# Optimization experiments

Hardware: AMD Instinct MI355X
Metric: run time of the kernel (lower is better)

The kernel has to match this reference:

```python
import jax, jax.numpy as jnp
import numpy as np

BS, C, H, W = 8, 128, 64, 64
CH = C // 2  # proj output channels


def setup_inputs() -> dict:
    key = jax.random.key(0)
    ks = jax.random.split(key, 8)
    s = 1.0 / np.sqrt(C)
    return {
        "tgt": jax.random.normal(ks[0], (BS, C, H, W), dtype=jnp.float32),
        "ref": jax.random.normal(ks[1], (BS, C, H, W), dtype=jnp.float32),
        "W_tgt": jax.random.normal(ks[2], (CH, C), dtype=jnp.float32) * s,
        "b_tgt": jax.random.normal(ks[3], (CH,), dtype=jnp.float32) * s,
        "W_ref": jax.random.normal(ks[4], (CH, C), dtype=jnp.float32) * s,
        "b_ref": jax.random.normal(ks[5], (CH,), dtype=jnp.float32) * s,
        "W_out": jax.random.normal(ks[6], (C, C), dtype=jnp.float32) * s,
        "b_out": jax.random.normal(ks[7], (C,), dtype=jnp.float32) * s,
    }


def reference(tgt, ref, W_tgt, b_tgt, W_ref, b_ref, W_out, b_out):
    bs, c, h, w = tgt.shape
    n = h * w
    # 1x1 conv == per-pixel matmul over channels; flatten spatial to tokens
    tgt_f = tgt.reshape(bs, c, n)              # [bs, c, n]
    ref_f = ref.reshape(bs, c, n)              # [bs, c, n]
    # att_tgt: [bs, n, c/2] ; att_ref: [bs, c/2, n] (ReLU after proj)
    att_tgt = jax.nn.relu(jnp.einsum('bcn,oc->bno', tgt_f, W_tgt) + b_tgt)
    att_ref = jax.nn.relu(jnp.einsum('bcn,oc->bon', ref_f, W_ref) + b_ref[None, :, None])
    pre_att = jnp.einsum('bnd,bdm->bnm', att_tgt, att_ref)   # [bs, n, n]
    att = jax.nn.softmax(pre_att, axis=-1)
    # fused tokens: [bs, n, c] = att @ ref_tokens
    fused = jnp.einsum('bnm,bcm->bnc', att, ref_f)
    fused = fused.transpose(0, 2, 1).reshape(bs, c, h, w)
    # output gate: 1x1 conv on tgt (no activation), elementwise mul
    att_out = jnp.einsum('bcn,oc->bon', tgt_f, W_out) + b_out[None, :, None]
    fused = fused * att_out.reshape(bs, c, h, w)
    return fused
```

## Files before the change

### kernel.cpp

```cpp
#include <hip/hip_runtime.h>

typedef __attribute__((ext_vector_type(8))) _Float16 f16x8;
typedef __attribute__((ext_vector_type(4))) float f32x4;
typedef __attribute__((ext_vector_type(16))) float f32x16;
typedef __attribute__((ext_vector_type(2))) unsigned u32x2;

constexpr int kC  = 128;
constexpr int kCH = 64;
constexpr int kN  = 4096;
constexpr float kLog2e = 1.4426950408889634f;

__device__ __forceinline__ unsigned pkrtz(float a, float b) {
    union { __fp16 __attribute__((ext_vector_type(2))) v; unsigned u; } cv;
    cv.v = __builtin_amdgcn_cvt_pkrtz(a, b);
    return cv.u;
}

__device__ __forceinline__ float x2(float x) {
    return __builtin_amdgcn_exp2f(x);
}

__device__ __forceinline__ float hadd2(unsigned u) {
    union { unsigned v; _Float16 h[2]; } c; c.v = u;
    return (float)c.h[0] + (float)c.h[1];
}

__device__ __forceinline__ u32x2 pl32(unsigned a, unsigned b) {
    return __builtin_amdgcn_permlane32_swap(a, b, false, false);
}
__device__ __forceinline__ u32x2 pl32x(float v) {
    float c;
    asm("v_mov_b32 %0, %1" : "=&v"(c) : "v"(v));
    union { float f; unsigned u; } a, b2; a.f = v; b2.f = c;
    return pl32(a.u, b2.u);
}
__device__ __forceinline__ float uf(unsigned u) {
    union { unsigned v; float f; } c; c.v = u; return c.f;
}

__device__ __forceinline__ void g2l16(const unsigned short* g, unsigned short* l) {
    __builtin_amdgcn_global_load_lds(
        (const __attribute__((address_space(1))) unsigned int*)(g),
        (__attribute__((address_space(3))) unsigned int*)(l),
        16, 0, 0);
}

__global__ __launch_bounds__(256, 2) void proj_fused(
    const float* __restrict__ tgt, const float* __restrict__ ref,
    const float* __restrict__ Wt, const float* __restrict__ Wr,
    const float* __restrict__ Wo, const float* __restrict__ bt,
    const float* __restrict__ br, const float* __restrict__ bo,
    unsigned short* __restrict__ Qw, unsigned short* __restrict__ Kw,
    unsigned short* __restrict__ Vw, float* __restrict__ Gw)
{
    __shared__ __align__(16) unsigned short Xs[2][64 * 128];
    const int t = threadIdx.x;
    const int sl2 = blockIdx.y >> 3;
    const int b = blockIdx.y & 7;
    const int tok0 = blockIdx.x << 7;

    const int w = t >> 6, lane = t & 63;
    const int lg = (lane >> 4) & 3, lm = lane & 15;

    const float* X = sl2 ? ref : tgt;
    const float* Xb0 = X + ((size_t)b * kC) * kN + tok0;
    unsigned short* Vout = Vw + ((size_t)b * kC) * kN + tok0;

    const float* Wqk  = sl2 ? Wr : Wt;
    const float* bqk  = sl2 ? br : bt;
    const float scale = sl2 ? 1.0f : kLog2e;

    f16x8 wfq[4];
    float bq[4];
    {
        const int ocb = w * 16;
        #pragma unroll
        for (int ks = 0; ks < 4; ++ks) {
            const float* wp = Wqk + (size_t)(ocb + lm) * kC + ks * 32 + lg * 8;
            f32x4 f0 = *(const f32x4*)wp;
            f32x4 f1 = *(const f32x4*)(wp + 4);
            union { f16x8 h; uint4 u; } cv;
            cv.u = make_uint4(pkrtz(f0[0] * scale, f0[1] * scale),
                              pkrtz(f0[2] * scale, f0[3] * scale),
                              pkrtz(f1[0] * scale, f1[1] * scale),
                              pkrtz(f1[2] * scale, f1[3] * scale));
            wfq[ks] = cv.h;
        }
        #pragma unroll
        for (int r = 0; r < 4; ++r) bq[r] = bqk[ocb + lg * 4 + r] * scale;
    }

    f16x8 wfg[2][4];
    float bg[2][4];
    if (sl2 == 0) {
        const int ocb = w * 32;
        #pragma unroll
        for (int ot = 0; ot < 2; ++ot) {
            const int oc = ocb + ot * 16 + lm;
            #pragma unroll
            for (int ks = 0; ks < 4; ++ks) {
                const float* wp = Wo + (size_t)oc * kC + ks * 32 + lg * 8;
                f32x4 f0 = *(const f32x4*)wp;
                f32x4 f1 = *(const f32x4*)(wp + 4);
                union { f16x8 h; uint4 u; } cv;
                cv.u = make_uint4(pkrtz(f0[0], f0[1]), pkrtz(f0[2], f0[3]),
                                  pkrtz(f1[0], f1[1]), pkrtz(f1[2], f1[3]));
                wfg[ot][ks] = cv.h;
            }
            #pragma unroll
            for (int r = 0; r < 4; ++r) bg[ot][r] = bo[ocb + ot * 16 + lg * 4 + r];
        }
    }

    const int tk4 = (t & 15) * 4;
    const int c8  = (t >> 4) * 8;

    auto loadX = [&](int toff, f32x4* xv) {
        #pragma unroll
        for (int j = 0; j < 8; ++j)
            xv[j] = *(const f32x4*)(Xb0 + (size_t)(c8 + j) * kN + toff + tk4);
    };
    auto stageX = [&](const f32x4* xv, unsigned short* Xsb, int toff) {
        if (sl2 == 1) {
            #pragma unroll
            for (int j = 0; j < 8; ++j)
                *(uint2*)(Vout + (size_t)(c8 + j) * kN + toff + tk4) =
                    make_uint2(pkrtz(xv[j][0], xv[j][1]), pkrtz(xv[j][2], xv[j][3]));
        }
        #pragma unroll
        for (int s = 0; s < 4; ++s) {
            const int tok = tk4 + s;
            const int cc = (c8 >> 3) ^ (tok & 7);
            uint4 pk;
            pk.x = pkrtz(xv[0][s], xv[1][s]);
            pk.y = pkrtz(xv[2][s], xv[3][s]);
            pk.z = pkrtz(xv[4][s], xv[5][s]);
            pk.w = pkrtz(xv[6][s], xv[7][s]);
            *(uint4*)(Xsb + tok * 128 + cc * 8) = pk;
        }
    };
    auto compute = [&](const unsigned short* Xsb, int tokb) {
        unsigned short* outp = (sl2 ? Kw : Qw) + ((size_t)b * kN + tokb) * kCH;
        float* Gb = Gw + ((size_t)b * kC) * kN + tokb;
        const int ocq = w * 16;
        const int ocg = w * 32;
        #pragma unroll
        for (int ns = 0; ns < 4; ++ns) {
            const int tok = ns * 16 + lm;
            f16x8 xf[4];
            #pragma unroll
            for (int ks = 0; ks < 4; ++ks)
                xf[ks] = *(const f16x8*)(Xsb + tok * 128 +
                                         (((ks * 4 + lg) ^ (tok & 7)) << 3));
            {
                f32x4 acc = {bq[0], bq[1], bq[2], bq[3]};
                #pragma unroll
                for (int ks = 0; ks < 4; ++ks)
                    acc = __builtin_amdgcn_mfma_f32_16x16x32_f16(wfq[ks], xf[ks], acc, 0, 0, 0);
                uint2 pk;
                pk.x = pkrtz(fmaxf(acc[0], 0.f), fmaxf(acc[1], 0.f));
                pk.y = pkrtz(fmaxf(acc[2], 0.f), fmaxf(acc[3], 0.f));
                *(uint2*)(outp + (size_t)tok * kCH + ocq + lg * 4) = pk;
            }
            if (sl2 == 0) {
                #pragma unroll
                for (int ot = 0; ot < 2; ++ot) {
                    f32x4 acc = {bg[ot][0], bg[ot][1], bg[ot][2], bg[ot][3]};
                    #pragma unroll
                    for (int ks = 0; ks < 4; ++ks)
                        acc = __builtin_amdgcn_mfma_f32_16x16x32_f16(wfg[ot][ks], xf[ks], acc, 0, 0, 0);
                    #pragma unroll
                    for (int r = 0; r < 4; ++r)
                        Gb[(size_t)(ocg + ot * 16 + lg * 4 + r) * kN + tok] = acc[r];
                }
            }
        }
    };

    f32x4 xv[8], xw[8];
    loadX(0, xv);
    stageX(xv, Xs[0], 0);
    __syncthreads();
    loadX(64, xw);
    compute(Xs[0], tok0);
    stageX(xw, Xs[1], 64);
    __syncthreads();
    compute(Xs[1], tok0 + 64);
}

__global__ __launch_bounds__(256, 2) void flash12_kernel(
    const unsigned short* __restrict__ Qw,
    const unsigned short* __restrict__ Kw,
    const unsigned short* __restrict__ Vw,
    const float* __restrict__ Gw,
    float* __restrict__ out)
{
    __shared__ __align__(16) unsigned short Ks[2][64 * 64];
    __shared__ __align__(16) unsigned short Vs[3][128 * 64];
    __shared__ float2 mlb[4][32];

    const int t = threadIdx.x;
    const int b  = blockIdx.x & 7;
    const int n0 = (blockIdx.x >> 3) << 6;
    const int w = t >> 6, lane = t & 63;
    const int qg = w >> 1, kh = w & 1;
    const int lq = lane & 31, hh = lane >> 5;
    const int n0q = n0 + qg * 32 + lq;

    const unsigned short* Qb = Qw + ((size_t)b * kN + n0q) * kCH;
    const unsigned short* Kb = Kw + ((size_t)b * kN) * kCH;
    const unsigned short* Vb = Vw + ((size_t)b * kC) * kN;

    f16x8 qf[4];
    #pragma unroll
    for (int st = 0; st < 4; ++st)
        qf[st] = *(const f16x8*)(Qb + st * 16 + hh * 8);

    const int srow = t >> 3, scol = t & 7;
    const int sco  = (scol ^ (srow & 7)) << 3;
    const int wv   = t >> 6;

    int ka[4];
    #pragma unroll
    for (int st = 0; st < 4; ++st)
        ka[st] = (kh * 32 + lq) * 64 + (((2 * st + hh) ^ (lq & 7)) << 3);
    int va[4][2];
    #pragma unroll
    for (int cb = 0; cb < 4; ++cb)
        #pragma unroll
        for (int s = 0; s < 2; ++s)
            va[cb][s] = (cb * 32 + lq) * 64 + (((kh * 4 + 2 * s + hh) ^ (lq & 7)) << 3);

    f32x16 O[4];
    #pragma unroll
    for (int cb = 0; cb < 4; ++cb)
        #pragma unroll
        for (int r = 0; r < 16; ++r) O[cb][r] = 0.f;
    float L = 0.f, m_run = 0.f;

    f16x8 pfp[2];
    {
        union { uint4 u; f16x8 h; } z;
        z.u = make_uint4(0u, 0u, 0u, 0u);
        pfp[0] = z.h; pfp[1] = z.h;
    }

    auto stage = [&](unsigned short* Kd, unsigned short* Vd, int m0) {
        g2l16(Kb + (size_t)(m0 + srow) * kCH + sco,      Kd + wv * 512);
        g2l16(Kb + (size_t)(m0 + 32 + srow) * kCH + sco, Kd + 2048 + wv * 512);
        #pragma unroll
        for (int j = 0; j < 4; ++j)
            g2l16(Vb + (size_t)(32 * j + srow) * kN + m0 + sco,
                  Vd + j * 2048 + wv * 512);
    };

    unsigned short *Kt = Ks[0], *Kn = Ks[1];
    unsigned short *Vp = Vs[2], *Vt = Vs[0], *Vn = Vs[1];
    stage(Kt, Vt, 0);

    for (int kt = 0; kt < kN / 64; ++kt) {
        __syncthreads();
        if (kt + 1 < kN / 64) stage(Kn, Vn, (kt + 1) << 6);

        f32x16 sa;
        #pragma unroll
        for (int r = 0; r < 16; ++r) sa[r] = 0.f;
        __builtin_amdgcn_s_setprio(1);
        #pragma unroll
        for (int st = 0; st < 4; ++st) {
            f16x8 kf = *(const f16x8*)(Kt + ka[st]);
            sa = __builtin_amdgcn_mfma_f32_32x32x16_f16(kf, qf[st], sa, 0, 0, 0);
        }
        __builtin_amdgcn_s_setprio(0);

        float mh = sa[0];
        #pragma unroll
        for (int r = 1; r < 16; ++r) mh = fmaxf(mh, sa[r]);
        u32x2 mr = pl32x(mh);
        const float mq = fmaxf(uf(mr[0]), uf(mr[1]));
        const bool resc = __any(mq > m_run + 8.0f);
        const float mnew = resc ? fmaxf(m_run, mq) : m_run;

        __builtin_amdgcn_s_setprio(1);
        if (kt > 0) {
            #pragma unroll
            for (int cb = 0; cb < 4; ++cb) {
                #pragma unroll
                for (int s = 0; s < 2; ++s) {
                    f16x8 vf = *(const f16x8*)(Vp + va[cb][s]);
                    O[cb] = __builtin_amdgcn_mfma_f32_32x32x16_f16(vf, pfp[s], O[cb], 0, 0, 0);
                }
            }
        }
        __builtin_amdgcn_s_setprio(0);

        #pragma unroll
        for (int r = 0; r < 16; ++r) sa[r] = x2(sa[r] - mnew);
        unsigned P[8];
        #pragma unroll
        for (int i = 0; i < 8; ++i) P[i] = pkrtz(sa[2 * i], sa[2 * i + 1]);
        float ps = 0.f;
        #pragma unroll
        for (int i = 0; i < 8; ++i) ps += hadd2(P[i]);
        u32x2 pr = pl32x(ps);
        ps = uf(pr[0]) + uf(pr[1]);

        if (resc) {
            const float al = x2(m_run - mnew);
            #pragma unroll
            for (int cb = 0; cb < 4; ++cb) O[cb] *= al;
            L = L * al + ps;
            m_run = mnew;
        } else {
            L += ps;
        }

        #pragma unroll
        for (int s = 0; s < 2; ++s) {
            u32x2 r0 = pl32(P[4 * s + 0], P[4 * s + 2]);
            u32x2 r1 = pl32(P[4 * s + 1], P[4 * s + 3]);
            union { uint4 u; f16x8 h; } cv;
            cv.u = make_uint4(r0[0], r1[0], r0[1], r1[1]);
            pfp[s] = cv.h;
        }

        unsigned short* tv = Vp; Vp = Vt; Vt = Vn; Vn = tv;
        unsigned short* tk = Kt; Kt = Kn; Kn = tk;
    }

    __builtin_amdgcn_s_setprio(1);
    #pragma unroll
    for (int cb = 0; cb < 4; ++cb) {
        #pragma unroll
        for (int s = 0; s < 2; ++s) {
            f16x8 vf = *(const f16x8*)(Vp + va[cb][s]);
            O[cb] = __builtin_amdgcn_mfma_f32_32x32x16_f16(vf, pfp[s], O[cb], 0, 0, 0);
        }
    }
    __builtin_amdgcn_s_setprio(0);

    __syncthreads();
    mlb[w][lq] = make_float2(m_run, L);
    __syncthreads();
    const float2 pml = mlb[w ^ 1][lq];
    const float mt = fmaxf(m_run, pml.x);
    const float a  = x2(m_run - mt);
    const float Lt = L * a + pml.y * x2(pml.x - mt);

    float* Obuf = (float*)Vs;
    const int obase = qg * 4096 + lane * 64;
    #pragma unroll
    for (int cb = 0; cb < 4; ++cb) O[cb] *= a;

    if (kh) {
        #pragma unroll
        for (int c = 0; c < 16; ++c) {
            const int cb = c >> 2, q4 = c & 3;
            *(float4*)(Obuf + obase + (((c + lane) & 15) << 2)) =
                make_float4(O[cb][q4 * 4 + 0], O[cb][q4 * 4 + 1],
                            O[cb][q4 * 4 + 2], O[cb][q4 * 4 + 3]);
        }
    }
    __syncthreads();
    if (!kh) {
        #pragma unroll
        for (int c = 0; c < 16; ++c) {
            const int cb = c >> 2, q4 = c & 3;
            float4 p = *(const float4*)(Obuf + obase + (((c + lane) & 15) << 2));
            O[cb][q4 * 4 + 0] += p.x;
            O[cb][q4 * 4 + 1] += p.y;
            O[cb][q4 * 4 + 2] += p.z;
            O[cb][q4 * 4 + 3] += p.w;
        }
        const float inv = 1.0f / Lt;
        const float* Gb = Gw + ((size_t)b * kC + 4 * hh) * kN + n0 + qg * 32 + lq;
        float*       Ob = out + ((size_t)b * kC + 4 * hh) * kN + n0 + qg * 32 + lq;
        #pragma unroll
        for (int cb = 0; cb < 4; ++cb) {
            #pragma unroll
            for (int r = 0; r < 16; ++r) {
                const int coff = cb * 32 + (r & 3) + 8 * (r >> 2);
                Ob[(size_t)coff * kN] = O[cb][r] * inv * Gb[(size_t)coff * kN];
            }
        }
    }
}

extern "C" void kernel_launch(void* const* d_in, const int* in_sizes, int n_in,
                              void* d_out, int out_size, void* d_ws, size_t ws_size,
                              hipStream_t stream) {
    const float* tgt   = (const float*)d_in[0];
    const float* ref   = (const float*)d_in[1];
    const float* W_tgt = (const float*)d_in[2];
    const float* b_tgt = (const float*)d_in[3];
    const float* W_ref = (const float*)d_in[4];
    const float* b_ref = (const float*)d_in[5];
    const float* W_out = (const float*)d_in[6];
    const float* b_out = (const float*)d_in[7];
    float* out = (float*)d_out;

    const size_t QK = (size_t)8 * kN * kCH;
    const size_t CV = (size_t)8 * kC * kN;
    unsigned short* Qw = (unsigned short*)d_ws;
    unsigned short* Kw = Qw + QK;
    unsigned short* Vw = Kw + QK;
    float*          Gw = (float*)(Vw + CV);

    proj_fused<<<dim3(32, 16), 256, 0, stream>>>(tgt, ref, W_tgt, W_ref, W_out,
                                                 b_tgt, b_ref, b_out, Qw, Kw, Vw, Gw);
    flash12_kernel<<<dim3(512), 256, 0, stream>>>(Qw, Kw, Vw, Gw, out);
}
```

Measured before the change: 174.6 us.

## Load K/V fragments directly into registers instead of LDS staging

The attention kernel no longer stages K and V tiles through shared memory with global_load_lds and per-tile __syncthreads. Each wave now loads its own MFMA fragments straight from global memory into register double buffers, one tile ahead, with the loop unrolled by two to alternate buffers. The row-max is rewritten as a tree reduction and the probability row-sum uses packed fp16 adds. This removes LDS traffic and block barriers, but raises register pressure, duplicates global loads across waves that share K, uses less coalesced V accesses, and accumulates partial sums at lower precision.

```diff
diff --git a/kernel.cpp b/kernel.cpp
--- a/kernel.cpp
+++ b/kernel.cpp
@@ -1,6 +1,7 @@
 #include <hip/hip_runtime.h>
 
 typedef __attribute__((ext_vector_type(8))) _Float16 f16x8;
+typedef __attribute__((ext_vector_type(2))) _Float16 h2;
 typedef __attribute__((ext_vector_type(4))) float f32x4;
 typedef __attribute__((ext_vector_type(16))) float f32x16;
 typedef __attribute__((ext_vector_type(2))) unsigned u32x2;
@@ -20,9 +21,8 @@
     return __builtin_amdgcn_exp2f(x);
 }
 
-__device__ __forceinline__ float hadd2(unsigned u) {
-    union { unsigned v; _Float16 h[2]; } c; c.v = u;
-    return (float)c.h[0] + (float)c.h[1];
+__device__ __forceinline__ h2 uh(unsigned u) {
+    union { unsigned v; h2 h; } c; c.v = u; return c.h;
 }
 
 __device__ __forceinline__ u32x2 pl32(unsigned a, unsigned b) {
@@ -36,13 +36,6 @@
 }
 __device__ __forceinline__ float uf(unsigned u) {
     union { unsigned v; float f; } c; c.v = u; return c.f;
-}
-
-__device__ __forceinline__ void g2l16(const unsigned short* g, unsigned short* l) {
-    __builtin_amdgcn_global_load_lds(
-        (const __attribute__((address_space(1))) unsigned int*)(g),
-        (__attribute__((address_space(3))) unsigned int*)(l),
-        16, 0, 0);
 }
 
 __global__ __launch_bounds__(256, 2) void proj_fused(
@@ -188,15 +181,14 @@
     compute(Xs[1], tok0 + 64);
 }
 
-__global__ __launch_bounds__(256, 2) void flash12_kernel(
+__global__ __launch_bounds__(256, 2) void flash13_kernel(
     const unsigned short* __restrict__ Qw,
     const unsigned short* __restrict__ Kw,
     const unsigned short* __restrict__ Vw,
     const float* __restrict__ Gw,
     float* __restrict__ out)
 {
-    __shared__ __align__(16) unsigned short Ks[2][64 * 64];
-    __shared__ __align__(16) unsigned short Vs[3][128 * 64];
+    __shared__ __align__(16) float Obuf[8192];
     __shared__ float2 mlb[4][32];
 
     const int t = threadIdx.x;
@@ -206,30 +198,16 @@
     const int qg = w >> 1, kh = w & 1;
     const int lq = lane & 31, hh = lane >> 5;
     const int n0q = n0 + qg * 32 + lq;
+    constexpr int NT = kN / 64;
 
     const unsigned short* Qb = Qw + ((size_t)b * kN + n0q) * kCH;
-    const unsigned short* Kb = Kw + ((size_t)b * kN) * kCH;
-    const unsigned short* Vb = Vw + ((size_t)b * kC) * kN;
+    const unsigned short* Kr = Kw + ((size_t)b * kN + kh * 32 + lq) * kCH + hh * 8;
+    const unsigned short* Vr = Vw + ((size_t)b * kC + lq) * (size_t)kN + kh * 32 + hh * 8;
 
     f16x8 qf[4];
     #pragma unroll
     for (int st = 0; st < 4; ++st)
         qf[st] = *(const f16x8*)(Qb + st * 16 + hh * 8);
-
-    const int srow = t >> 3, scol = t & 7;
-    const int sco  = (scol ^ (srow & 7)) << 3;
-    const int wv   = t >> 6;
-
-    int ka[4];
-    #pragma unroll
-    for (int st = 0; st < 4; ++st)
-        ka[st] = (kh * 32 + lq) * 64 + (((2 * st + hh) ^ (lq & 7)) << 3);
-    int va[4][2];
-    #pragma unroll
-    for (int cb = 0; cb < 4; ++cb)
-        #pragma unroll
-        for (int s = 0; s < 2; ++s)
-            va[cb][s] = (cb * 32 + lq) * 64 + (((kh * 4 + 2 * s + hh) ^ (lq & 7)) << 3);
 
     f32x16 O[4];
     #pragma unroll
@@ -245,37 +223,42 @@
         pfp[0] = z.h; pfp[1] = z.h;
     }
 
-    auto stage = [&](unsigned short* Kd, unsigned short* Vd, int m0) {
-        g2l16(Kb + (size_t)(m0 + srow) * kCH + sco,      Kd + wv * 512);
-        g2l16(Kb + (size_t)(m0 + 32 + srow) * kCH + sco, Kd + 2048 + wv * 512);
-        #pragma unroll
-        for (int j = 0; j < 4; ++j)
-            g2l16(Vb + (size_t)(32 * j + srow) * kN + m0 + sco,
-                  Vd + j * 2048 + wv * 512);
-    };
-
-    unsigned short *Kt = Ks[0], *Kn = Ks[1];
-    unsigned short *Vp = Vs[2], *Vt = Vs[0], *Vn = Vs[1];
-    stage(Kt, Vt, 0);
-
-    for (int kt = 0; kt < kN / 64; ++kt) {
-        __syncthreads();
-        if (kt + 1 < kN / 64) stage(Kn, Vn, (kt + 1) << 6);
+    auto loadK = [&](f16x8 (&Kd)[4], int m0) {
+        #pragma unroll
+        for (int st = 0; st < 4; ++st)
+            Kd[st] = *(const f16x8*)(Kr + (size_t)m0 * kCH + st * 16);
+    };
+    auto loadV = [&](f16x8 (&Vd)[4][2], int m0) {
+        #pragma unroll
+        for (int cb = 0; cb < 4; ++cb)
+            #pragma unroll
+            for (int s = 0; s < 2; ++s)
+                Vd[cb][s] = *(const f16x8*)(Vr + (size_t)cb * 32 * kN + m0 + s * 16);
+    };
+
+    f16x8 KA[4], KB[4], VA[4][2], VB[4][2];
+    loadK(KA, 0);
+
+    auto tile = [&](f16x8 (&Kc)[4], f16x8 (&Kn)[4],
+                    f16x8 (&Vc)[4][2], f16x8 (&Vp)[4][2], int kt) {
+        const int m0 = kt << 6;
+        loadV(Vc, m0);
+        if (kt + 1 < NT) loadK(Kn, m0 + 64);
 
         f32x16 sa;
         #pragma unroll
         for (int r = 0; r < 16; ++r) sa[r] = 0.f;
         __builtin_amdgcn_s_setprio(1);
         #pragma unroll
-        for (int st = 0; st < 4; ++st) {
-            f16x8 kf = *(const f16x8*)(Kt + ka[st]);
-            sa = __builtin_amdgcn_mfma_f32_32x32x16_f16(kf, qf[st], sa, 0, 0, 0);
-        }
+        for (int st = 0; st < 4; ++st)
+            sa = __builtin_amdgcn_mfma_f32_32x32x16_f16(Kc[st], qf[st], sa, 0, 0, 0);
         __builtin_amdgcn_s_setprio(0);
 
-        float mh = sa[0];
-        #pragma unroll
-        for (int r = 1; r < 16; ++r) mh = fmaxf(mh, sa[r]);
+        float m0a = fmaxf(fmaxf(sa[0], sa[1]), fmaxf(sa[2], sa[3]));
+        float m0b = fmaxf(fmaxf(sa[4], sa[5]), fmaxf(sa[6], sa[7]));
+        float m0c = fmaxf(fmaxf(sa[8], sa[9]), fmaxf(sa[10], sa[11]));
+        float m0d = fmaxf(fmaxf(sa[12], sa[13]), fmaxf(sa[14], sa[15]));
+        float mh = fmaxf(fmaxf(m0a, m0b), fmaxf(m0c, m0d));
         u32x2 mr = pl32x(mh);
         const float mq = fmaxf(uf(mr[0]), uf(mr[1]));
         const bool resc = __any(mq > m_run + 8.0f);
@@ -286,10 +269,8 @@
             #pragma unroll
             for (int cb = 0; cb < 4; ++cb) {
                 #pragma unroll
-                for (int s = 0; s < 2; ++s) {
-                    f16x8 vf = *(const f16x8*)(Vp + va[cb][s]);
-                    O[cb] = __builtin_amdgcn_mfma_f32_32x32x16_f16(vf, pfp[s], O[cb], 0, 0, 0);
-                }
+                for (int s = 0; s < 2; ++s)
+                    O[cb] = __builtin_amdgcn_mfma_f32_32x32x16_f16(Vp[cb][s], pfp[s], O[cb], 0, 0, 0);
             }
         }
         __builtin_amdgcn_s_setprio(0);
@@ -299,9 +280,12 @@
         unsigned P[8];
         #pragma unroll
         for (int i = 0; i < 8; ++i) P[i] = pkrtz(sa[2 * i], sa[2 * i + 1]);
-        float ps = 0.f;
-        #pragma unroll
-        for (int i = 0; i < 8; ++i) ps += hadd2(P[i]);
+        h2 s0 = uh(P[0]) + uh(P[1]);
+        h2 s1 = uh(P[2]) + uh(P[3]);
+        h2 s2 = uh(P[4]) + uh(P[5]);
+        h2 s3 = uh(P[6]) + uh(P[7]);
+        s0 += s1; s2 += s3; s0 += s2;
+        float ps = (float)s0[0] + (float)s0[1];
         u32x2 pr = pl32x(ps);
         ps = uf(pr[0]) + uf(pr[1]);
 
@@ -323,19 +307,19 @@
             cv.u = make_uint4(r0[0], r1[0], r0[1], r1[1]);
             pfp[s] = cv.h;
         }
-
-        unsigned short* tv = Vp; Vp = Vt; Vt = Vn; Vn = tv;
-        unsigned short* tk = Kt; Kt = Kn; Kn = tk;
+    };
+
+    for (int kt = 0; kt < NT; kt += 2) {
+        tile(KA, KB, VA, VB, kt);
+        tile(KB, KA, VB, VA, kt + 1);
     }
 
     __builtin_amdgcn_s_setprio(1);
     #pragma unroll
     for (int cb = 0; cb < 4; ++cb) {
         #pragma unroll
-        for (int s = 0; s < 2; ++s) {
-            f16x8 vf = *(const f16x8*)(Vp + va[cb][s]);
-            O[cb] = __builtin_amdgcn_mfma_f32_32x32x16_f16(vf, pfp[s], O[cb], 0, 0, 0);
-        }
+        for (int s = 0; s < 2; ++s)
+            O[cb] = __builtin_amdgcn_mfma_f32_32x32x16_f16(VB[cb][s], pfp[s], O[cb], 0, 0, 0);
     }
     __builtin_amdgcn_s_setprio(0);
 
@@ -347,7 +331,6 @@
     const float a  = x2(m_run - mt);
     const float Lt = L * a + pml.y * x2(pml.x - mt);
 
-    float* Obuf = (float*)Vs;
     const int obase = qg * 4096 + lane * 64;
     #pragma unroll
     for (int cb = 0; cb < 4; ++cb) O[cb] *= a;
@@ -408,5 +391,5 @@
 
     proj_fused<<<dim3(32, 16), 256, 0, stream>>>(tgt, ref, W_tgt, W_ref, W_out,
                                                  b_tgt, b_ref, b_out, Qw, Kw, Vw, Gw);
-    flash12_kernel<<<dim3(512), 256, 0, stream>>>(Qw, Kw, Vw, Gw, out);
-}
+    flash13_kernel<<<dim3(512), 256, 0, stream>>>(Qw, Kw, Vw, Gw, out);
+}
```

New measurement: 271.9 us. +55.7%, slower.

## Double flash block to 512 threads covering 128 queries, sharing K/V tiles

Applied to the files above, without the earlier changes.

The attention kernel now runs 512-thread blocks, each handling 128 query rows instead of 64, with half as many blocks. Each K/V tile staged into LDS is therefore reused by twice as many waves, which halves global K/V traffic per query. The LDS is merged into a single byte buffer carved into K, V and reduction regions, and staging is redistributed over the larger thread count. The row-max and probability-sum reductions become trees, with the sum done in packed fp16 adds, which shortens dependency chains but accumulates the partial sums in lower precision.

```diff
diff --git a/kernel.cpp b/kernel.cpp
--- a/kernel.cpp
+++ b/kernel.cpp
@@ -1,6 +1,7 @@
 #include <hip/hip_runtime.h>
 
 typedef __attribute__((ext_vector_type(8))) _Float16 f16x8;
+typedef __attribute__((ext_vector_type(2))) _Float16 h2;
 typedef __attribute__((ext_vector_type(4))) float f32x4;
 typedef __attribute__((ext_vector_type(16))) float f32x16;
 typedef __attribute__((ext_vector_type(2))) unsigned u32x2;
@@ -20,9 +21,8 @@
     return __builtin_amdgcn_exp2f(x);
 }
 
-__device__ __forceinline__ float hadd2(unsigned u) {
-    union { unsigned v; _Float16 h[2]; } c; c.v = u;
-    return (float)c.h[0] + (float)c.h[1];
+__device__ __forceinline__ h2 uh(unsigned u) {
+    union { unsigned v; h2 h; } c; c.v = u; return c.h;
 }
 
 __device__ __forceinline__ u32x2 pl32(unsigned a, unsigned b) {
@@ -188,24 +188,23 @@
     compute(Xs[1], tok0 + 64);
 }
 
-__global__ __launch_bounds__(256, 2) void flash12_kernel(
+__global__ __launch_bounds__(512, 4) void flash14_kernel(
     const unsigned short* __restrict__ Qw,
     const unsigned short* __restrict__ Kw,
     const unsigned short* __restrict__ Vw,
     const float* __restrict__ Gw,
     float* __restrict__ out)
 {
-    __shared__ __align__(16) unsigned short Ks[2][64 * 64];
-    __shared__ __align__(16) unsigned short Vs[3][128 * 64];
-    __shared__ float2 mlb[4][32];
+    __shared__ __align__(16) unsigned char SM[67584];
 
     const int t = threadIdx.x;
     const int b  = blockIdx.x & 7;
-    const int n0 = (blockIdx.x >> 3) << 6;
+    const int n0 = (blockIdx.x >> 3) << 7;
     const int w = t >> 6, lane = t & 63;
     const int qg = w >> 1, kh = w & 1;
     const int lq = lane & 31, hh = lane >> 5;
     const int n0q = n0 + qg * 32 + lq;
+    constexpr int NT = kN / 64;
 
     const unsigned short* Qb = Qw + ((size_t)b * kN + n0q) * kCH;
     const unsigned short* Kb = Kw + ((size_t)b * kN) * kCH;
@@ -246,21 +245,23 @@
     }
 
     auto stage = [&](unsigned short* Kd, unsigned short* Vd, int m0) {
-        g2l16(Kb + (size_t)(m0 + srow) * kCH + sco,      Kd + wv * 512);
-        g2l16(Kb + (size_t)(m0 + 32 + srow) * kCH + sco, Kd + 2048 + wv * 512);
-        #pragma unroll
-        for (int j = 0; j < 4; ++j)
-            g2l16(Vb + (size_t)(32 * j + srow) * kN + m0 + sco,
-                  Vd + j * 2048 + wv * 512);
+        g2l16(Kb + (size_t)(m0 + srow) * kCH + sco, Kd + wv * 512);
+        #pragma unroll
+        for (int j = 0; j < 2; ++j)
+            g2l16(Vb + (size_t)(64 * j + srow) * kN + m0 + sco,
+                  Vd + j * 4096 + wv * 512);
     };
 
-    unsigned short *Kt = Ks[0], *Kn = Ks[1];
-    unsigned short *Vp = Vs[2], *Vt = Vs[0], *Vn = Vs[1];
+    unsigned short *Kt = (unsigned short*)SM;
+    unsigned short *Kn = (unsigned short*)(SM + 8192);
+    unsigned short *Vp = (unsigned short*)(SM + 49152);
+    unsigned short *Vt = (unsigned short*)(SM + 16384);
+    unsigned short *Vn = (unsigned short*)(SM + 32768);
     stage(Kt, Vt, 0);
 
-    for (int kt = 0; kt < kN / 64; ++kt) {
+    for (int kt = 0; kt < NT; ++kt) {
         __syncthreads();
-        if (kt + 1 < kN / 64) stage(Kn, Vn, (kt + 1) << 6);
+        if (kt + 1 < NT) stage(Kn, Vn, (kt + 1) << 6);
 
         f32x16 sa;
         #pragma unroll
@@ -273,9 +274,11 @@
         }
         __builtin_amdgcn_s_setprio(0);
 
-        float mh = sa[0];
-        #pragma unroll
-        for (int r = 1; r < 16; ++r) mh = fmaxf(mh, sa[r]);
+        float m0a = fmaxf(fmaxf(sa[0], sa[1]), fmaxf(sa[2], sa[3]));
+        float m0b = fmaxf(fmaxf(sa[4], sa[5]), fmaxf(sa[6], sa[7]));
+        float m0c = fmaxf(fmaxf(sa[8], sa[9]), fmaxf(sa[10], sa[11]));
+        float m0d = fmaxf(fmaxf(sa[12], sa[13]), fmaxf(sa[14], sa[15]));
+        float mh = fmaxf(fmaxf(m0a, m0b), fmaxf(m0c, m0d));
         u32x2 mr = pl32x(mh);
         const float mq = fmaxf(uf(mr[0]), uf(mr[1]));
         const bool resc = __any(mq > m_run + 8.0f);
@@ -299,9 +302,12 @@
         unsigned P[8];
         #pragma unroll
         for (int i = 0; i < 8; ++i) P[i] = pkrtz(sa[2 * i], sa[2 * i + 1]);
-        float ps = 0.f;
-        #pragma unroll
-        for (int i = 0; i < 8; ++i) ps += hadd2(P[i]);
+        h2 s0 = uh(P[0]) + uh(P[1]);
+        h2 s1 = uh(P[2]) + uh(P[3]);
+        h2 s2 = uh(P[4]) + uh(P[5]);
+        h2 s3 = uh(P[6]) + uh(P[7]);
+        s0 += s1; s2 += s3; s0 += s2;
+        float ps = (float)s0[0] + (float)s0[1];
         u32x2 pr = pl32x(ps);
         ps = uf(pr[0]) + uf(pr[1]);
 
@@ -339,15 +345,16 @@
     }
     __builtin_amdgcn_s_setprio(0);
 
+    float2* mlb = (float2*)(SM + 65536);
     __syncthreads();
-    mlb[w][lq] = make_float2(m_run, L);
+    mlb[w * 32 + lq] = make_float2(m_run, L);
     __syncthreads();
-    const float2 pml = mlb[w ^ 1][lq];
+    const float2 pml = mlb[(w ^ 1) * 32 + lq];
     const float mt = fmaxf(m_run, pml.x);
     const float a  = x2(m_run - mt);
     const float Lt = L * a + pml.y * x2(pml.x - mt);
 
-    float* Obuf = (float*)Vs;
+    float* Obuf = (float*)SM;
     const int obase = qg * 4096 + lane * 64;
     #pragma unroll
     for (int cb = 0; cb < 4; ++cb) O[cb] *= a;
@@ -408,5 +415,5 @@
 
     proj_fused<<<dim3(32, 16), 256, 0, stream>>>(tgt, ref, W_tgt, W_ref, W_out,
                                                  b_tgt, b_ref, b_out, Qw, Kw, Vw, Gw);
-    flash12_kernel<<<dim3(512), 256, 0, stream>>>(Qw, Kw, Vw, Gw, out);
-}
+    flash14_kernel<<<dim3(256), 512, 0, stream>>>(Qw, Kw, Vw, Gw, out);
+}
```

After: 163.7 us. -6.2%, faster.
